# Performance work log

Measured on AMD Instinct MI355X. Metric: run time of the kernel, lower is better.

Reference implementation:

```python
import jax, jax.numpy as jnp
import numpy as np

DEFOCUS_MAX = 4.0
R_MAX = int(DEFOCUS_MAX) + 1   # matches kernel's intRadius = int(fltRadius) + 1 at max defocus
GAMMA = 4.0                    # tanh sharpness of the soft disk edge
PI = 3.141592653589793


def setup_inputs():
    key = jax.random.key(0)
    k1, k2 = jax.random.split(key)
    B, C, H, W = 2, 3, 512, 512
    image = jax.random.uniform(k1, (B, C, H, W), dtype=jnp.float32)
    # signed per-pixel circle-of-confusion radius, scaled to [0, DEFOCUS_MAX)
    defocus = jax.random.uniform(k2, (B, 1, H, W), dtype=jnp.float32) * DEFOCUS_MAX
    return {"image": image, "defocus": defocus}


def _render(image, defocus):
    # Scatter form (CUDA kernel): every source pixel p splats w(p, dist) * image[p]
    # into all q with |q-p|_inf <= int(|defocus[p]|)+1, plus w into weight_cum.
    # Equivalent gather form used here: out[q] = sum over offsets o of
    # w(q-o, |o|) * image[q-o], vectorized over all pixels per offset.
    B, C, H, W = image.shape
    R = R_MAX
    r = jnp.abs(defocus)                              # CoC radius per source pixel
    int_r = jnp.floor(r) + 1.0                        # square scatter window half-size
    inv_area = 1.0 / jnp.maximum(PI * r * r, 1.0)     # disk-area normalization

    pad = ((0, 0), (0, 0), (R, R), (R, R))
    img_p = jnp.pad(image, pad)
    r_p = jnp.pad(r, pad)
    ir_p = jnp.pad(int_r, pad)
    inv_p = jnp.pad(inv_area, pad)
    val_p = jnp.pad(jnp.ones((B, 1, H, W), jnp.float32), pad)  # in-bounds source mask

    offs = np.stack(np.meshgrid(np.arange(-R, R + 1), np.arange(-R, R + 1),
                                indexing='ij'), -1).reshape(-1, 2)
    offs = jnp.asarray(offs, jnp.int32)               # ((2R+1)^2, 2)

    def body(carry, off):
        bokeh, wsum = carry
        dy, dx = off[0], off[1]
        y0, x0 = R - dy, R - dx                       # source p = q - (dy, dx)
        src_img = jax.lax.dynamic_slice(img_p, (0, 0, y0, x0), (B, C, H, W))
        src_r = jax.lax.dynamic_slice(r_p, (0, 0, y0, x0), (B, 1, H, W))
        src_ir = jax.lax.dynamic_slice(ir_p, (0, 0, y0, x0), (B, 1, H, W))
        src_inv = jax.lax.dynamic_slice(inv_p, (0, 0, y0, x0), (B, 1, H, W))
        src_val = jax.lax.dynamic_slice(val_p, (0, 0, y0, x0), (B, 1, H, W))
        dist = jnp.sqrt((dy * dy + dx * dx).astype(jnp.float32))
        in_win = (jnp.abs(dy).astype(jnp.float32) <= src_ir) & \
                 (jnp.abs(dx).astype(jnp.float32) <= src_ir)
        w = (0.5 + 0.5 * jnp.tanh(GAMMA * (src_r - dist))) * src_inv
        w = jnp.where(in_win, w, 0.0) * src_val
        return (bokeh + w * src_img, wsum + w), None

    init = (jnp.zeros((B, C, H, W), jnp.float32),
            jnp.zeros((B, 1, H, W), jnp.float32))
    (bokeh_cum, weight_cum), _ = jax.lax.scan(jax.checkpoint(body), init, offs)
    return bokeh_cum / weight_cum


def reference(image, defocus):
    return _render(image, defocus)
```

## Files before the change

### kernel.cpp

```cpp
#include <hip/hip_runtime.h>
#include <cmath>


#define HH 512
#define WW 512
#define NB 2
#define TW 64
#define TH 16
#define HALO 4
#define SROWS (TH + 2 * HALO)
#define LW 72

__device__ __forceinline__ unsigned rtne_hi(float v) {
  unsigned u = __float_as_uint(v);
  u = u + 0x7FFFu + ((u >> 16) & 1u);
  return u & 0xFFFF0000u;
}

__global__ __launch_bounds__(512, 4) void bokeh_gather(
    const float* __restrict__ img,
    const float* __restrict__ def,
    float* __restrict__ out)
{
  __shared__ __align__(16) unsigned sX[SROWS][LW];
  __shared__ __align__(16) unsigned sY[SROWS][LW];
  __shared__ __align__(16) unsigned sZ[SROWS][LW];
  __shared__ float sFd[9][12];
  __shared__ __align__(16) float pbuf[256][20];

  const int tid = threadIdx.x;
  const int s   = tid >> 8;
  const int t   = tid & 255;
  const int tx  = t & 15;
  const int ty  = t >> 4;
  const int bx = blockIdx.x * TW;
  const int by = blockIdx.y * TH;
  const int b  = blockIdx.z;

  if (tid < 81) {
    int dyi = tid / 9, dxi = tid - dyi * 9;
    int dyo = dyi - 4, dxo = dxi - 4;
    float d2 = (float)(dyo * dyo + dxo * dxo);
    sFd[dyi][dxi] = __expf(8.0f * sqrtf(d2));
  }

  const float* dpt = def + b * (HH * WW);
  const float* ipt = img + b * (3 * HH * WW);

  for (int idx = tid; idx < SROWS * LW; idx += 512) {
    int ly = idx / LW;
    int lx = idx - ly * LW;
    int sy = by - HALO + ly;
    int sx = bx - HALO + lx;
    unsigned X = 0u, Y = 0u, Z = 0u;
    if ((unsigned)sy < (unsigned)HH && (unsigned)sx < (unsigned)WW) {
      int o = sy * WW + sx;
      float r = fabsf(dpt[o]);
      float G  = __expf(-8.0f * r);
      float iv = __builtin_amdgcn_rcpf(fmaxf(3.14159265358979f * r * r, 1.0f));
      X = rtne_hi(G) | (rtne_hi(iv) >> 16);
      Y = rtne_hi(ipt[o]) | (rtne_hi(ipt[o + HH * WW]) >> 16);
      Z = __float_as_uint(ipt[o + 2 * HH * WW]) & 0xFFFF0000u;
    }
    sX[ly][lx] = X;
    sY[ly][lx] = Y;
    sZ[ly][lx] = Z;
  }
  __syncthreads();

  float wsum[4] = {0.f, 0.f, 0.f, 0.f};
  float ac0[4]  = {0.f, 0.f, 0.f, 0.f};
  float ac1[4]  = {0.f, 0.f, 0.f, 0.f};
  float ac2[4]  = {0.f, 0.f, 0.f, 0.f};

  const int col0 = 4 * tx;
  const int dy0 = s ? 5 : 0;
  const int dy1 = s ? 9 : 5;

  #pragma unroll 1
  for (int dy = dy0; dy < dy1; ++dy) {
    const int sr = ty + dy;
    float fdr[9];
    #pragma unroll
    for (int x = 0; x < 9; ++x) fdr[x] = sFd[dy][x];

    unsigned Xv[12], Yv[12], Zv[12];
    #pragma unroll
    for (int q = 0; q < 3; ++q) {
      *(uint4*)&Xv[4 * q] = *(const uint4*)(&sX[sr][col0] + 4 * q);
      *(uint4*)&Yv[4 * q] = *(const uint4*)(&sY[sr][col0] + 4 * q);
      *(uint4*)&Zv[4 * q] = *(const uint4*)(&sZ[sr][col0] + 4 * q);
    }
    float Gv[12], Iv[12], C0[12], C1[12];
    #pragma unroll
    for (int j = 0; j < 12; ++j) {
      Gv[j] = __uint_as_float(Xv[j] & 0xFFFF0000u);
      Iv[j] = __uint_as_float(Xv[j] << 16);
      C0[j] = __uint_as_float(Yv[j] & 0xFFFF0000u);
      C1[j] = __uint_as_float(Yv[j] << 16);
    }

    #pragma unroll
    for (int k = 0; k < 4; ++k) {
      #pragma unroll
      for (int j = k; j < k + 9; ++j) {
        const int xi = j - k;
        float tden = fmaf(Gv[j], fdr[xi], 1.0f);
        float w = __builtin_amdgcn_rcpf(tden) * Iv[j];
        wsum[k] += w;
        ac0[k] = fmaf(w, C0[j], ac0[k]);
        ac1[k] = fmaf(w, C1[j], ac1[k]);
        ac2[k] = fmaf(w, __uint_as_float(Zv[j]), ac2[k]);
      }
    }
  }

  if (s == 1) {
    float4 v0 = {wsum[0], wsum[1], wsum[2], wsum[3]};
    float4 v1 = {ac0[0], ac0[1], ac0[2], ac0[3]};
    float4 v2 = {ac1[0], ac1[1], ac1[2], ac1[3]};
    float4 v3 = {ac2[0], ac2[1], ac2[2], ac2[3]};
    *(float4*)&pbuf[t][0]  = v0;
    *(float4*)&pbuf[t][4]  = v1;
    *(float4*)&pbuf[t][8]  = v2;
    *(float4*)&pbuf[t][12] = v3;
  }
  __syncthreads();
  if (s == 0) {
    float4 v0 = *(const float4*)&pbuf[t][0];
    float4 v1 = *(const float4*)&pbuf[t][4];
    float4 v2 = *(const float4*)&pbuf[t][8];
    float4 v3 = *(const float4*)&pbuf[t][12];
    wsum[0] += v0.x; wsum[1] += v0.y; wsum[2] += v0.z; wsum[3] += v0.w;
    ac0[0] += v1.x; ac0[1] += v1.y; ac0[2] += v1.z; ac0[3] += v1.w;
    ac1[0] += v2.x; ac1[1] += v2.y; ac1[2] += v2.z; ac1[3] += v2.w;
    ac2[0] += v3.x; ac2[1] += v3.y; ac2[2] += v3.z; ac2[3] += v3.w;

    const int oy = by + ty;
    const int ox = bx + col0;
    float rw[4];
    #pragma unroll
    for (int k = 0; k < 4; ++k) rw[k] = __builtin_amdgcn_rcpf(wsum[k]);

    float* op0 = out + ((b * 3 + 0) * HH + oy) * WW + ox;
    float* op1 = out + ((b * 3 + 1) * HH + oy) * WW + ox;
    float* op2 = out + ((b * 3 + 2) * HH + oy) * WW + ox;
    float4 o0, o1, o2;
    o0.x = ac0[0] * rw[0]; o0.y = ac0[1] * rw[1]; o0.z = ac0[2] * rw[2]; o0.w = ac0[3] * rw[3];
    o1.x = ac1[0] * rw[0]; o1.y = ac1[1] * rw[1]; o1.z = ac1[2] * rw[2]; o1.w = ac1[3] * rw[3];
    o2.x = ac2[0] * rw[0]; o2.y = ac2[1] * rw[1]; o2.z = ac2[2] * rw[2]; o2.w = ac2[3] * rw[3];
    *(float4*)op0 = o0;
    *(float4*)op1 = o1;
    *(float4*)op2 = o2;
  }
}

extern "C" void kernel_launch(void* const* d_in, const int* in_sizes, int n_in,
                              void* d_out, int out_size, void* d_ws, size_t ws_size,
                              hipStream_t stream) {
  const float* img = (const float*)d_in[0];
  const float* def = (const float*)d_in[1];
  float* out = (float*)d_out;

  dim3 grid(WW / TW, HH / TH, NB);
  dim3 block(512);
  hipLaunchKernelGGL(bokeh_gather, grid, block, 0, stream, img, def, out);
}
```

Measured before the change: 19.36 us.

## Split dy loop across four thread groups with 1024-thread blocks

Doubles the block size to 1024 threads and splits the 9 dy rows among four 256-thread groups instead of two. Partial sums are chained through shared memory with two extra barrier stages before the final normalization. The aim is to shorten the per-thread serial loop and add waves per CU for latency hiding. The risks are tighter register limits from the launch bounds and extra synchronization, and the last group still carries 3 of the 9 rows.

```diff
diff --git a/kernel.cpp b/kernel.cpp
--- a/kernel.cpp
+++ b/kernel.cpp
@@ -17,7 +17,7 @@
   return u & 0xFFFF0000u;
 }
 
-__global__ __launch_bounds__(512, 4) void bokeh_gather(
+__global__ __launch_bounds__(1024, 8) void bokeh_gather(
     const float* __restrict__ img,
     const float* __restrict__ def,
     float* __restrict__ out)
@@ -47,7 +47,7 @@
   const float* dpt = def + b * (HH * WW);
   const float* ipt = img + b * (3 * HH * WW);
 
-  for (int idx = tid; idx < SROWS * LW; idx += 512) {
+  for (int idx = tid; idx < SROWS * LW; idx += 1024) {
     int ly = idx / LW;
     int lx = idx - ly * LW;
     int sy = by - HALO + ly;
@@ -74,8 +74,8 @@
   float ac2[4]  = {0.f, 0.f, 0.f, 0.f};
 
   const int col0 = 4 * tx;
-  const int dy0 = s ? 5 : 0;
-  const int dy1 = s ? 9 : 5;
+  const int dy0 = (s == 0) ? 0 : (s == 1) ? 2 : (s == 2) ? 4 : 6;
+  const int dy1 = (s == 0) ? 2 : (s == 1) ? 4 : (s == 2) ? 6 : 9;
 
   #pragma unroll 1
   for (int dy = dy0; dy < dy1; ++dy) {
@@ -116,14 +116,32 @@
   }
 
   if (s == 1) {
-    float4 v0 = {wsum[0], wsum[1], wsum[2], wsum[3]};
-    float4 v1 = {ac0[0], ac0[1], ac0[2], ac0[3]};
-    float4 v2 = {ac1[0], ac1[1], ac1[2], ac1[3]};
-    float4 v3 = {ac2[0], ac2[1], ac2[2], ac2[3]};
-    *(float4*)&pbuf[t][0]  = v0;
-    *(float4*)&pbuf[t][4]  = v1;
-    *(float4*)&pbuf[t][8]  = v2;
-    *(float4*)&pbuf[t][12] = v3;
+    *(float4*)&pbuf[t][0]  = make_float4(wsum[0], wsum[1], wsum[2], wsum[3]);
+    *(float4*)&pbuf[t][4]  = make_float4(ac0[0], ac0[1], ac0[2], ac0[3]);
+    *(float4*)&pbuf[t][8]  = make_float4(ac1[0], ac1[1], ac1[2], ac1[3]);
+    *(float4*)&pbuf[t][12] = make_float4(ac2[0], ac2[1], ac2[2], ac2[3]);
+  }
+  __syncthreads();
+  if (s == 2) {
+    float4 v0 = *(const float4*)&pbuf[t][0];
+    float4 v1 = *(const float4*)&pbuf[t][4];
+    float4 v2 = *(const float4*)&pbuf[t][8];
+    float4 v3 = *(const float4*)&pbuf[t][12];
+    *(float4*)&pbuf[t][0]  = make_float4(v0.x + wsum[0], v0.y + wsum[1], v0.z + wsum[2], v0.w + wsum[3]);
+    *(float4*)&pbuf[t][4]  = make_float4(v1.x + ac0[0], v1.y + ac0[1], v1.z + ac0[2], v1.w + ac0[3]);
+    *(float4*)&pbuf[t][8]  = make_float4(v2.x + ac1[0], v2.y + ac1[1], v2.z + ac1[2], v2.w + ac1[3]);
+    *(float4*)&pbuf[t][12] = make_float4(v3.x + ac2[0], v3.y + ac2[1], v3.z + ac2[2], v3.w + ac2[3]);
+  }
+  __syncthreads();
+  if (s == 3) {
+    float4 v0 = *(const float4*)&pbuf[t][0];
+    float4 v1 = *(const float4*)&pbuf[t][4];
+    float4 v2 = *(const float4*)&pbuf[t][8];
+    float4 v3 = *(const float4*)&pbuf[t][12];
+    *(float4*)&pbuf[t][0]  = make_float4(v0.x + wsum[0], v0.y + wsum[1], v0.z + wsum[2], v0.w + wsum[3]);
+    *(float4*)&pbuf[t][4]  = make_float4(v1.x + ac0[0], v1.y + ac0[1], v1.z + ac0[2], v1.w + ac0[3]);
+    *(float4*)&pbuf[t][8]  = make_float4(v2.x + ac1[0], v2.y + ac1[1], v2.z + ac1[2], v2.w + ac1[3]);
+    *(float4*)&pbuf[t][12] = make_float4(v3.x + ac2[0], v3.y + ac2[1], v3.z + ac2[2], v3.w + ac2[3]);
   }
   __syncthreads();
   if (s == 0) {
@@ -163,6 +181,6 @@
   float* out = (float*)d_out;
 
   dim3 grid(WW / TW, HH / TH, NB);
-  dim3 block(512);
+  dim3 block(1024);
   hipLaunchKernelGGL(bokeh_gather, grid, block, 0, stream, img, def, out);
 }
```

New measurement: 70.42 us. 264% more time.
